# Kernel optimization log

Hardware: AMD Instinct MI355X
Metric: run time of the kernel (lower is better)

The kernel has to match this reference:

```python
import jax, jax.numpy as jnp
import numpy as np


def setup_inputs() -> dict:
    key = jax.random.key(0)
    ks = jax.random.split(key, 8)
    B, C, H, W = 4, 256, 64, 64
    Ci = C // 8  # inter_channels = 32
    x = jax.random.normal(ks[0], (B, C, H, W), dtype=jnp.float32)
    # 1x1 conv weights stored as [out, in] matrices (kernel size 1)
    sq = 1.0 / np.sqrt(C)
    Wq = jax.random.uniform(ks[1], (Ci, C), jnp.float32, -sq, sq)
    bq = jax.random.uniform(ks[2], (Ci,), jnp.float32, -sq, sq)
    Wk = jax.random.uniform(ks[3], (Ci, C), jnp.float32, -sq, sq)
    bk = jax.random.uniform(ks[4], (Ci,), jnp.float32, -sq, sq)
    Wv = jax.random.uniform(ks[5], (C, C), jnp.float32, -sq, sq)
    bv = jax.random.uniform(ks[6], (C,), jnp.float32, -sq, sq)
    # torch initializes gamma to zeros; use a nonzero value so output depends on attention path
    gamma = jnp.array([0.5], dtype=jnp.float32)
    return {"x": x, "Wq": Wq, "bq": bq, "Wk": Wk, "bk": bk, "Wv": Wv, "bv": bv, "gamma": gamma}


def reference(x, Wq, bq, Wk, bk, Wv, bv, gamma):
    B, C, H, W = x.shape
    N = H * W
    xf = x.reshape(B, C, N)                        # [B, C, N]
    # 1x1 convs == channel-mixing matmuls
    q = jnp.einsum('oc,bcn->bon', Wq, xf) + bq[None, :, None]   # [B, Ci, N]
    k = jnp.einsum('oc,bcn->bon', Wk, xf) + bk[None, :, None]   # [B, Ci, N]
    v = jnp.einsum('oc,bcn->bon', Wv, xf) + bv[None, :, None]   # [B, C,  N]
    # energy[b, n, m] = sum_c q[b, c, n] * k[b, c, m]  (no scaling, per DANet)
    energy = jnp.einsum('bcn,bcm->bnm', q, k)      # [B, N, N]
    attention = jax.nn.softmax(energy, axis=-1)    # softmax over keys m
    # out[b, c, n] = sum_m v[b, c, m] * attention[b, n, m]
    out = jnp.einsum('bcm,bnm->bcn', v, attention)
    out = out.reshape(B, C, H, W)
    return gamma[0] * out + x
```

## Files before the change

### kernel.cpp

```cpp
#include <hip/hip_runtime.h>
#include <hip/hip_bf16.h>
#include <math.h>

typedef __bf16 bf16x8 __attribute__((ext_vector_type(8)));
typedef float  floatx4 __attribute__((ext_vector_type(4)));
typedef float  floatx16 __attribute__((ext_vector_type(16)));
typedef unsigned u32x2 __attribute__((ext_vector_type(2)));

#define MFMA(a, b, c)   __builtin_amdgcn_mfma_f32_16x16x32_bf16((a), (b), (c), 0, 0, 0)
#define MFMA32(a, b, c) __builtin_amdgcn_mfma_f32_32x32x16_bf16((a), (b), (c), 0, 0, 0)

__device__ __forceinline__ unsigned short f2bf(float f) {
  union { float f; unsigned u; } v; v.f = f;
  unsigned r = v.u + 0x7FFFu + ((v.u >> 16) & 1u);
  return (unsigned short)(r >> 16);
}
__device__ __forceinline__ float bf2f(unsigned short u) {
  union { unsigned u; float f; } v; v.u = ((unsigned)u) << 16;
  return v.f;
}
__device__ __forceinline__ unsigned pack2(float a, float b) {
  __bf16 x = (__bf16)a, y = (__bf16)b;
  unsigned short ux = __builtin_bit_cast(unsigned short, x);
  unsigned short uy = __builtin_bit_cast(unsigned short, y);
  return (unsigned)ux | ((unsigned)uy << 16);
}
__device__ __forceinline__ float exp2_fast(float x) {
#if __has_builtin(__builtin_amdgcn_exp2f)
  return __builtin_amdgcn_exp2f(x);
#else
  return exp2f(x);
#endif
}

__global__ __launch_bounds__(256) void k_wconv(const float* __restrict__ Wq,
                                               const float* __restrict__ Wk,
                                               const float* __restrict__ Wv,
                                               unsigned short* __restrict__ Wall) {
  int i = blockIdx.x * 256 + threadIdx.x;
  int o = i >> 8, c = i & 255;
  float v = (o < 32) ? Wq[o * 256 + c]
          : (o < 64) ? Wk[(o - 32) * 256 + c]
                     : Wv[(o - 64) * 256 + c];
  Wall[i] = f2bf(v);
}

__global__ __launch_bounds__(256) void k_projx(const float* __restrict__ x,
                                               const unsigned short* __restrict__ Wall,
                                               const float* __restrict__ bq,
                                               const float* __restrict__ bk,
                                               const float* __restrict__ bv,
                                               unsigned short* __restrict__ qbf,
                                               unsigned short* __restrict__ kbf,
                                               unsigned short* __restrict__ vbf) {
  int b = blockIdx.x >> 8;
  int m0 = (blockIdx.x & 255) * 16;
  int tid = threadIdx.x;
  int qr = tid >> 6;
  int lane = tid & 63;
  int l15 = lane & 15, quad = lane >> 4;

  __shared__ alignas(16) unsigned short xs[16][264];
  __shared__ alignas(16) unsigned short Os[4][64][24];

  {
    const float* xrow = x + ((size_t)b * 256 + tid) * 4096 + m0;
#pragma unroll
    for (int g = 0; g < 4; ++g) {
      float4 d = *(const float4*)(xrow + g * 4);
      xs[g * 4 + 0][tid] = f2bf(d.x);
      xs[g * 4 + 1][tid] = f2bf(d.y);
      xs[g * 4 + 2][tid] = f2bf(d.z);
      xs[g * 4 + 3][tid] = f2bf(d.w);
    }
  }
  __syncthreads();

  floatx4 acc[5];
#pragma unroll
  for (int tt = 0; tt < 5; ++tt) acc[tt] = floatx4{0.f, 0.f, 0.f, 0.f};

#pragma unroll
  for (int ks = 0; ks < 8; ++ks) {
    bf16x8 a = *(const bf16x8*)&xs[l15][ks * 32 + quad * 8];
    {
      bf16x8 w = *(const bf16x8*)(Wall + (size_t)(qr * 16 + l15) * 256 + ks * 32 + quad * 8);
      acc[0] = MFMA(a, w, acc[0]);
    }
#pragma unroll
    for (int t = 0; t < 4; ++t) {
      int gt = 4 + qr * 4 + t;
      bf16x8 w = *(const bf16x8*)(Wall + (size_t)(gt * 16 + l15) * 256 + ks * 32 + quad * 8);
      acc[1 + t] = MFMA(a, w, acc[1 + t]);
    }
  }
  {
    int o = qr * 16 + l15;
    float bias = (o < 32) ? bq[o] : bk[o - 32];
    float scale = (o < 32) ? 1.44269504088896340736f : 1.0f;
    unsigned short* dst = (o < 32) ? qbf : kbf;
    int oc = o & 31;
    int kh = oc >> 4, h2 = (oc >> 3) & 1, c8 = oc & 7;
#pragma unroll
    for (int r = 0; r < 4; ++r) {
      int m = m0 + quad * 4 + r;
      dst[(size_t)b * 131072 + (size_t)(m >> 5) * 1024 + kh * 512 + h2 * 256 +
          (m & 31) * 8 + c8] = f2bf((acc[0][r] + bias) * scale);
    }
  }
#pragma unroll
  for (int t = 0; t < 4; ++t) {
    int lr = t * 16 + l15;
    int c = qr * 64 + lr;
    float bias = bv[c];
#pragma unroll
    for (int r = 0; r < 4; ++r)
      Os[qr][lr][quad * 4 + r] = f2bf(acc[1 + t][r] + bias);
  }
  __syncthreads();
  {
    int kb = m0 >> 5, kk = (m0 >> 4) & 1;
#pragma unroll
    for (int i = 0; i < 2; ++i) {
      int idx = lane + 64 * i;
      int r = idx >> 1, g = idx & 1;
      int c = qr * 64 + r;
      int cb = c >> 5, ch = c & 31;
      *(uint4*)(vbf + (size_t)b * 1048576 + (size_t)kb * 8192 +
                (size_t)cb * 1024 + kk * 512 + g * 256 + ch * 8) =
          *(const uint4*)&Os[qr][r][g * 8];
    }
  }
}

__device__ __forceinline__ void softmax_pack(floatx16 st, float& lp, bf16x8 (&pa)[2], int hi) {
  float p[16];
#pragma unroll
  for (int r = 0; r < 16; ++r) p[r] = exp2_fast(st[r]);
  lp += (((p[0] + p[1]) + (p[2] + p[3])) + ((p[4] + p[5]) + (p[6] + p[7]))) +
        (((p[8] + p[9]) + (p[10] + p[11])) + ((p[12] + p[13]) + (p[14] + p[15])));
  unsigned d0[4], d1[4];
#pragma unroll
  for (int t = 0; t < 4; ++t) {
    d0[t] = pack2(p[4 * t + 0], p[4 * t + 1]);
    d1[t] = pack2(p[4 * t + 2], p[4 * t + 3]);
  }
#pragma unroll
  for (int ks = 0; ks < 2; ++ks) {
#if __has_builtin(__builtin_amdgcn_permlane32_swap)
    (void)hi;
    u32x2 r0 = __builtin_amdgcn_permlane32_swap(d0[2 * ks], d0[2 * ks + 1], false, false);
    u32x2 r1 = __builtin_amdgcn_permlane32_swap(d1[2 * ks], d1[2 * ks + 1], false, false);
    union { unsigned u[4]; bf16x8 v; } u;
    u.u[0] = r0[0]; u.u[1] = r1[0]; u.u[2] = r0[1]; u.u[3] = r1[1];
    pa[ks] = u.v;
#else
    unsigned s0 = hi ? d0[2 * ks] : d0[2 * ks + 1];
    unsigned s1 = hi ? d1[2 * ks] : d1[2 * ks + 1];
    unsigned o0 = (unsigned)__shfl_xor((int)s0, 32);
    unsigned o1 = (unsigned)__shfl_xor((int)s1, 32);
    union { unsigned u[4]; bf16x8 v; } u;
    u.u[0] = hi ? o0 : d0[2 * ks];
    u.u[1] = hi ? o1 : d1[2 * ks];
    u.u[2] = hi ? d0[2 * ks + 1] : o0;
    u.u[3] = hi ? d1[2 * ks + 1] : o1;
    pa[ks] = u.v;
#endif
  }
}

__global__ __launch_bounds__(64, 2) void k_attn(const unsigned short* __restrict__ qbf,
                                                const unsigned short* __restrict__ kbf,
                                                const unsigned short* __restrict__ vbf,
                                                unsigned short* __restrict__ Obf,
                                                float* __restrict__ lsum) {
  int wg = (blockIdx.x & 7) * 256 + (blockIdx.x >> 3);
  const int qb = wg & 127;
  const int g  = wg >> 7;
  const int s  = g & 3;
  const int b  = g >> 2;
  const int lane = threadIdx.x & 63;
  const int l31 = lane & 31;
  const int hi  = lane >> 5;
  const int q0  = qb * 32;

  const floatx16 z16 = {0.f, 0.f, 0.f, 0.f, 0.f, 0.f, 0.f, 0.f,
                        0.f, 0.f, 0.f, 0.f, 0.f, 0.f, 0.f, 0.f};

  bf16x8 qf[2];
  {
    const unsigned short* qbase =
        qbf + (size_t)b * 131072 + (size_t)qb * 1024 + hi * 256 + l31 * 8;
    qf[0] = *(const bf16x8*)(qbase);
    qf[1] = *(const bf16x8*)(qbase + 512);
  }

  floatx16 acc[8];
#pragma unroll
  for (int j = 0; j < 8; ++j) acc[j] = z16;

  float lp = 0.f;

  const unsigned short* krow =
      kbf + (size_t)b * 131072 + (size_t)(s * 32) * 1024 + hi * 256 + l31 * 8;
  const unsigned short* vrow =
      vbf + (size_t)b * 1048576 + (size_t)(s * 32) * 8192 + hi * 256 + l31 * 8;

  bf16x8 kf0 = *(const bf16x8*)krow;
  bf16x8 kf1 = *(const bf16x8*)(krow + 512);

  for (int it = 0; it < 32; ++it) {
    bf16x8 vb[8][2];
    const unsigned short* vit = vrow + (size_t)it * 8192;
#pragma unroll
    for (int cb = 0; cb < 8; ++cb) {
      vb[cb][0] = *(const bf16x8*)(vit + cb * 1024);
      vb[cb][1] = *(const bf16x8*)(vit + cb * 1024 + 512);
    }

    floatx16 st = MFMA32(kf0, qf[0], z16);
    st = MFMA32(kf1, qf[1], st);

    const unsigned short* kn = krow + (size_t)((it + 1) & 31) * 1024;
    kf0 = *(const bf16x8*)kn;
    kf1 = *(const bf16x8*)(kn + 512);

    bf16x8 pa[2];
    softmax_pack(st, lp, pa, hi);

    __builtin_amdgcn_s_setprio(1);
#pragma unroll
    for (int cb = 0; cb < 8; ++cb) {
      acc[cb] = MFMA32(pa[0], vb[cb][0], acc[cb]);
      acc[cb] = MFMA32(pa[1], vb[cb][1], acc[cb]);
    }
    __builtin_amdgcn_s_setprio(0);
  }

  lp += __shfl_xor(lp, 32);
  if (hi == 0) {
    lsum[((size_t)s * 4 + b) * 4096 + q0 + l31] = lp;
  }
#pragma unroll
  for (int cb = 0; cb < 8; ++cb) {
    unsigned short* orow = Obf +
        ((((size_t)s * 4 + b) * 128 + qb) * 256 + cb * 32 + l31) * 32 + hi * 4;
#pragma unroll
    for (int gi = 0; gi < 4; ++gi) {
      unsigned w0 = pack2(acc[cb][4 * gi + 0], acc[cb][4 * gi + 1]);
      unsigned w1 = pack2(acc[cb][4 * gi + 2], acc[cb][4 * gi + 3]);
      unsigned long long w = (unsigned long long)w0 | ((unsigned long long)w1 << 32);
      *(unsigned long long*)(orow + 8 * gi) = w;
    }
  }
}

__global__ __launch_bounds__(256) void k_merge(const unsigned short* __restrict__ Obf,
                                               const float* __restrict__ lsum,
                                               const float* __restrict__ x,
                                               const float* __restrict__ gma,
                                               float* __restrict__ out) {
  int t = blockIdx.x * 256 + threadIdx.x;
  int n4 = t & 1023;
  int c = (t >> 10) & 255;
  int b = t >> 18;
  int n = n4 << 2;
  int qb = n >> 5, off = n & 31;
  size_t xa = (((size_t)b * 256 + c) << 12) + n;
  float4 xv = *(const float4*)(x + xa);
  float L0 = 0.f, L1 = 0.f, L2 = 0.f, L3 = 0.f;
  float o0 = 0.f, o1 = 0.f, o2 = 0.f, o3 = 0.f;
#pragma unroll
  for (int s = 0; s < 4; ++s) {
    float4 ls = *(const float4*)(lsum + (((size_t)s * 4 + b) << 12) + n);
    L0 += ls.x; L1 += ls.y; L2 += ls.z; L3 += ls.w;
    ushort4 ov = *(const ushort4*)(
        Obf + ((((size_t)s * 4 + b) * 128 + qb) * 256 + c) * 32 + off);
    o0 += bf2f(ov.x); o1 += bf2f(ov.y); o2 += bf2f(ov.z); o3 += bf2f(ov.w);
  }
  float g = gma[0];
  float4 r;
  r.x = xv.x + g * o0 / L0;
  r.y = xv.y + g * o1 / L1;
  r.z = xv.z + g * o2 / L2;
  r.w = xv.w + g * o3 / L3;
  *(float4*)(out + xa) = r;
}

extern "C" void kernel_launch(void* const* d_in, const int* in_sizes, int n_in,
                              void* d_out, int out_size, void* d_ws, size_t ws_size,
                              hipStream_t stream) {
  const float* x   = (const float*)d_in[0];
  const float* Wq  = (const float*)d_in[1];
  const float* bq  = (const float*)d_in[2];
  const float* Wk  = (const float*)d_in[3];
  const float* bk  = (const float*)d_in[4];
  const float* Wv  = (const float*)d_in[5];
  const float* bv  = (const float*)d_in[6];
  const float* gma = (const float*)d_in[7];
  float* out = (float*)d_out;

  unsigned short* qbf  = (unsigned short*)d_ws;
  unsigned short* kbf  = qbf + (size_t)4 * 131072;
  unsigned short* vbf  = kbf + (size_t)4 * 131072;
  unsigned short* Wall = vbf + (size_t)4 * 1048576;
  unsigned short* Obf  = Wall + (size_t)320 * 256;
  float* lsum = (float*)(Obf + (size_t)4 * 4 * 256 * 4096);

  k_wconv<<<320, 256, 0, stream>>>(Wq, Wk, Wv, Wall);
  k_projx<<<1024, 256, 0, stream>>>(x, Wall, bq, bk, bv, qbf, kbf, vbf);
  k_attn<<<2048, 64, 0, stream>>>(qbf, kbf, vbf, Obf, lsum);
  k_merge<<<4096, 256, 0, stream>>>(Obf, lsum, x, gma, out);
}
```

Before: 180.1 us.

## Fuse split-key merge into attention kernel via shared-memory reduction

```diff
diff --git a/kernel.cpp b/kernel.cpp
--- a/kernel.cpp
+++ b/kernel.cpp
@@ -169,21 +169,27 @@
   }
 }
 
-__global__ __launch_bounds__(64, 2) void k_attn(const unsigned short* __restrict__ qbf,
-                                                const unsigned short* __restrict__ kbf,
-                                                const unsigned short* __restrict__ vbf,
-                                                unsigned short* __restrict__ Obf,
-                                                float* __restrict__ lsum) {
+__global__ __launch_bounds__(256, 4) void k_attn(const unsigned short* __restrict__ qbf,
+                                                 const unsigned short* __restrict__ kbf,
+                                                 const unsigned short* __restrict__ vbf,
+                                                 const float* __restrict__ x,
+                                                 const float* __restrict__ gma,
+                                                 float* __restrict__ out) {
   int wg = (blockIdx.x & 7) * 256 + (blockIdx.x >> 3);
   const int qb = wg & 127;
   const int g  = wg >> 7;
-  const int s  = g & 3;
+  const int cz = g & 3;
   const int b  = g >> 2;
+  const int s  = threadIdx.x >> 6;
   const int lane = threadIdx.x & 63;
   const int l31 = lane & 31;
   const int hi  = lane >> 5;
   const int q0  = qb * 32;
 
+  __shared__ float lpL[4][32];
+  __shared__ float ltot[32];
+  __shared__ alignas(16) unsigned short Ol[4][64][40];
+
   const floatx16 z16 = {0.f, 0.f, 0.f, 0.f, 0.f, 0.f, 0.f, 0.f,
                         0.f, 0.f, 0.f, 0.f, 0.f, 0.f, 0.f, 0.f};
 
@@ -195,27 +201,27 @@
     qf[1] = *(const bf16x8*)(qbase + 512);
   }
 
-  floatx16 acc[8];
-#pragma unroll
-  for (int j = 0; j < 8; ++j) acc[j] = z16;
+  floatx16 acc[2];
+  acc[0] = z16; acc[1] = z16;
 
   float lp = 0.f;
 
   const unsigned short* krow =
       kbf + (size_t)b * 131072 + (size_t)(s * 32) * 1024 + hi * 256 + l31 * 8;
   const unsigned short* vrow =
-      vbf + (size_t)b * 1048576 + (size_t)(s * 32) * 8192 + hi * 256 + l31 * 8;
+      vbf + (size_t)b * 1048576 + (size_t)(s * 32) * 8192 + (size_t)(cz * 2) * 1024 +
+      hi * 256 + l31 * 8;
 
   bf16x8 kf0 = *(const bf16x8*)krow;
   bf16x8 kf1 = *(const bf16x8*)(krow + 512);
 
   for (int it = 0; it < 32; ++it) {
-    bf16x8 vb[8][2];
+    bf16x8 vb[2][2];
     const unsigned short* vit = vrow + (size_t)it * 8192;
 #pragma unroll
-    for (int cb = 0; cb < 8; ++cb) {
-      vb[cb][0] = *(const bf16x8*)(vit + cb * 1024);
-      vb[cb][1] = *(const bf16x8*)(vit + cb * 1024 + 512);
+    for (int ct = 0; ct < 2; ++ct) {
+      vb[ct][0] = *(const bf16x8*)(vit + ct * 1024);
+      vb[ct][1] = *(const bf16x8*)(vit + ct * 1024 + 512);
     }
 
     floatx16 st = MFMA32(kf0, qf[0], z16);
@@ -230,61 +236,64 @@
 
     __builtin_amdgcn_s_setprio(1);
 #pragma unroll
-    for (int cb = 0; cb < 8; ++cb) {
-      acc[cb] = MFMA32(pa[0], vb[cb][0], acc[cb]);
-      acc[cb] = MFMA32(pa[1], vb[cb][1], acc[cb]);
+    for (int ct = 0; ct < 2; ++ct) {
+      acc[ct] = MFMA32(pa[0], vb[ct][0], acc[ct]);
+      acc[ct] = MFMA32(pa[1], vb[ct][1], acc[ct]);
     }
     __builtin_amdgcn_s_setprio(0);
   }
 
   lp += __shfl_xor(lp, 32);
-  if (hi == 0) {
-    lsum[((size_t)s * 4 + b) * 4096 + q0 + l31] = lp;
-  }
-#pragma unroll
-  for (int cb = 0; cb < 8; ++cb) {
-    unsigned short* orow = Obf +
-        ((((size_t)s * 4 + b) * 128 + qb) * 256 + cb * 32 + l31) * 32 + hi * 4;
+  if (hi == 0) lpL[s][l31] = lp;
+
+#pragma unroll
+  for (int ct = 0; ct < 2; ++ct) {
 #pragma unroll
     for (int gi = 0; gi < 4; ++gi) {
-      unsigned w0 = pack2(acc[cb][4 * gi + 0], acc[cb][4 * gi + 1]);
-      unsigned w1 = pack2(acc[cb][4 * gi + 2], acc[cb][4 * gi + 3]);
+      unsigned w0 = pack2(acc[ct][4 * gi + 0], acc[ct][4 * gi + 1]);
+      unsigned w1 = pack2(acc[ct][4 * gi + 2], acc[ct][4 * gi + 3]);
       unsigned long long w = (unsigned long long)w0 | ((unsigned long long)w1 << 32);
-      *(unsigned long long*)(orow + 8 * gi) = w;
-    }
-  }
-}
-
-__global__ __launch_bounds__(256) void k_merge(const unsigned short* __restrict__ Obf,
-                                               const float* __restrict__ lsum,
-                                               const float* __restrict__ x,
-                                               const float* __restrict__ gma,
-                                               float* __restrict__ out) {
-  int t = blockIdx.x * 256 + threadIdx.x;
-  int n4 = t & 1023;
-  int c = (t >> 10) & 255;
-  int b = t >> 18;
-  int n = n4 << 2;
-  int qb = n >> 5, off = n & 31;
-  size_t xa = (((size_t)b * 256 + c) << 12) + n;
-  float4 xv = *(const float4*)(x + xa);
-  float L0 = 0.f, L1 = 0.f, L2 = 0.f, L3 = 0.f;
-  float o0 = 0.f, o1 = 0.f, o2 = 0.f, o3 = 0.f;
-#pragma unroll
-  for (int s = 0; s < 4; ++s) {
-    float4 ls = *(const float4*)(lsum + (((size_t)s * 4 + b) << 12) + n);
-    L0 += ls.x; L1 += ls.y; L2 += ls.z; L3 += ls.w;
-    ushort4 ov = *(const ushort4*)(
-        Obf + ((((size_t)s * 4 + b) * 128 + qb) * 256 + c) * 32 + off);
-    o0 += bf2f(ov.x); o1 += bf2f(ov.y); o2 += bf2f(ov.z); o3 += bf2f(ov.w);
-  }
-  float g = gma[0];
-  float4 r;
-  r.x = xv.x + g * o0 / L0;
-  r.y = xv.y + g * o1 / L1;
-  r.z = xv.z + g * o2 / L2;
-  r.w = xv.w + g * o3 / L3;
-  *(float4*)(out + xa) = r;
+      *(unsigned long long*)&Ol[s][ct * 32 + l31][8 * gi + 4 * hi] = w;
+    }
+  }
+  __syncthreads();
+  if (threadIdx.x < 32) {
+    int q = threadIdx.x;
+    ltot[q] = (lpL[0][q] + lpL[1][q]) + (lpL[2][q] + lpL[3][q]);
+  }
+  __syncthreads();
+
+  {
+    const float gv = gma[0];
+    int ch = threadIdx.x >> 2;
+    int qg = threadIdx.x & 3;
+    float o[8];
+#pragma unroll
+    for (int j = 0; j < 8; ++j) o[j] = 0.f;
+#pragma unroll
+    for (int sp = 0; sp < 4; ++sp) {
+      uint4 a0 = *(const uint4*)&Ol[sp][ch][qg * 8];
+      unsigned uu[4] = {a0.x, a0.y, a0.z, a0.w};
+#pragma unroll
+      for (int jj = 0; jj < 4; ++jj) {
+        o[2 * jj + 0] += bf2f((unsigned short)(uu[jj] & 0xffffu));
+        o[2 * jj + 1] += bf2f((unsigned short)(uu[jj] >> 16));
+      }
+    }
+    size_t rowa = ((size_t)b * 256 + cz * 64 + ch) * 4096 + q0 + qg * 8;
+    const float* xrow = x + rowa;
+    float* orow = out + rowa;
+#pragma unroll
+    for (int j4 = 0; j4 < 2; ++j4) {
+      float4 xv = *(const float4*)(xrow + j4 * 4);
+      float4 r;
+      r.x = xv.x + gv * o[j4 * 4 + 0] / ltot[qg * 8 + j4 * 4 + 0];
+      r.y = xv.y + gv * o[j4 * 4 + 1] / ltot[qg * 8 + j4 * 4 + 1];
+      r.z = xv.z + gv * o[j4 * 4 + 2] / ltot[qg * 8 + j4 * 4 + 2];
+      r.w = xv.w + gv * o[j4 * 4 + 3] / ltot[qg * 8 + j4 * 4 + 3];
+      *(float4*)(orow + j4 * 4) = r;
+    }
+  }
 }
 
 extern "C" void kernel_launch(void* const* d_in, const int* in_sizes, int n_in,
@@ -304,11 +313,8 @@
   unsigned short* kbf  = qbf + (size_t)4 * 131072;
   unsigned short* vbf  = kbf + (size_t)4 * 131072;
   unsigned short* Wall = vbf + (size_t)4 * 1048576;
-  unsigned short* Obf  = Wall + (size_t)320 * 256;
-  float* lsum = (float*)(Obf + (size_t)4 * 4 * 256 * 4096);
 
   k_wconv<<<320, 256, 0, stream>>>(Wq, Wk, Wv, Wall);
   k_projx<<<1024, 256, 0, stream>>>(x, Wall, bq, bk, bv, qbf, kbf, vbf);
-  k_attn<<<2048, 64, 0, stream>>>(qbf, kbf, vbf, Obf, lsum);
-  k_merge<<<4096, 256, 0, stream>>>(Obf, lsum, x, gma, out);
-}
+  k_attn<<<2048, 256, 0, stream>>>(qbf, kbf, vbf, x, gma, out);
+}
```

New measurement: 177.5 us. Within noise of the previous version (-1.5%).
